# Performance work log

Measured on AMD Instinct MI355X. Metric: run time of the kernel, lower is better.

The kernel has to match this reference:

```python
import jax, jax.numpy as jnp
import numpy as np

# Bit-slice widths from SliceMethod([1,2,4]) on both input and weight sides
# (MSB-first, 7 magnitude bits total, sign carried per-element in each slice).
IN_SLICES = (1, 2, 4)
W_SLICES = (1, 2, 4)


def _l2norm(a):
    # F.normalize(a, p=2, dim=1)
    n = jnp.sqrt(jnp.sum(a * a, axis=1, keepdims=True))
    return a / jnp.maximum(n, 1e-12)


def _quantize(a, nbits):
    # symmetric fixed-point quantization to `nbits` magnitude bits,
    # dynamic per-tensor scale (bw_e=None -> fixed-point path)
    Q = float(2 ** nbits - 1)
    scale = jnp.max(jnp.abs(a))
    q = jnp.round(a / scale * Q)  # integer-valued float32 in [-Q, Q]
    return q, scale / Q


def _bit_slices(q, widths):
    # split |q| into bit groups (MSB-first per slice_method order); sign is
    # folded into each slice so recombination sum_k 2^off_k * slice_k == q
    sign = jnp.sign(q)
    mag = jnp.abs(q)
    total = sum(widths)
    slices = []
    off = total
    for w in widths:
        off -= w
        s = jnp.mod(jnp.floor(mag / (2.0 ** off)), 2.0 ** w)
        slices.append((sign * s, off))
    return slices


def setup_inputs() -> dict:
    key = jax.random.key(0)
    kx, kw = jax.random.split(key)
    x = jax.random.normal(kx, (4096, 1024), dtype=jnp.float32)
    weight = jax.random.normal(kw, (8192, 1024), dtype=jnp.float32)  # vectors.t -> [M, D]
    return {"x": x, "weight": weight}


def reference(x, weight):
    xn = _l2norm(x)        # [B, D]
    wn = _l2norm(weight)   # [M, D]
    qx, sx = _quantize(xn, sum(IN_SLICES))
    qw, sw = _quantize(wn, sum(W_SLICES))
    x_slices = _bit_slices(qx, IN_SLICES)
    w_slices = _bit_slices(qw, W_SLICES)
    # map_reduce_dot_func: 9 slice-pair low-bit GEMMs, recombined with 2^(oi+oj)
    acc = jnp.zeros((x.shape[0], weight.shape[0]), dtype=jnp.float32)
    for xs_k, ox in x_slices:
        for ws_k, ow in w_slices:
            acc = acc + (2.0 ** (ox + ow)) * jnp.einsum('bd,md->bm', xs_k, ws_k)
    cos = acc * sx * sw  # dequantize -> cosine similarity in [-1, 1]
    return 1.0 - cos
```

## Files before the change

kernel.cpp:

```cpp
#include <hip/hip_runtime.h>
#include <cstdint>
#include <cstddef>


#define D_COLS 1024
#define M_ROWS 4096
#define N_ROWS 8192

using i32x4 = __attribute__((ext_vector_type(4))) int;

__device__ __forceinline__ void gload_lds16(const void* g, void* lds) {
  __builtin_amdgcn_global_load_lds(
      (const __attribute__((address_space(1))) uint32_t*)g,
      (__attribute__((address_space(3))) uint32_t*)lds, 16, 0, 0);
}

__global__ __launch_bounds__(256) void rownorm_kernel(
    const float* __restrict__ x, const float* __restrict__ w,
    float* __restrict__ invnorm, float* __restrict__ rmax) {
  const int row = blockIdx.x;
  const float* a = (row < M_ROWS) ? x + (size_t)row * D_COLS
                                  : w + (size_t)(row - M_ROWS) * D_COLS;
  const float4 v = ((const float4*)a)[threadIdx.x];
  float ss = v.x * v.x + v.y * v.y + v.z * v.z + v.w * v.w;
  float mx = fmaxf(fmaxf(fabsf(v.x), fabsf(v.y)), fmaxf(fabsf(v.z), fabsf(v.w)));
#pragma unroll
  for (int off = 32; off; off >>= 1) {
    ss += __shfl_down(ss, off, 64);
    mx = fmaxf(mx, __shfl_down(mx, off, 64));
  }
  __shared__ float s_ss[4], s_mx[4];
  const int wave = threadIdx.x >> 6, lane = threadIdx.x & 63;
  if (lane == 0) { s_ss[wave] = ss; s_mx[wave] = mx; }
  __syncthreads();
  if (threadIdx.x == 0) {
    float tss = (s_ss[0] + s_ss[1]) + (s_ss[2] + s_ss[3]);
    float tmx = fmaxf(fmaxf(s_mx[0], s_mx[1]), fmaxf(s_mx[2], s_mx[3]));
    float inv = 1.0f / fmaxf(sqrtf(tss), 1e-12f);
    invnorm[row] = inv;
    rmax[row] = tmx * inv;
  }
}

__global__ __launch_bounds__(1024) void scale_reduce_kernel(
    const float* __restrict__ rmax, float* __restrict__ scales) {
  const int t = threadIdx.x;
  float mx = 0.f, mw = 0.f;
  for (int i = t; i < M_ROWS; i += 1024) mx = fmaxf(mx, rmax[i]);
  for (int i = t; i < N_ROWS; i += 1024) mw = fmaxf(mw, rmax[M_ROWS + i]);
#pragma unroll
  for (int off = 32; off; off >>= 1) {
    mx = fmaxf(mx, __shfl_down(mx, off, 64));
    mw = fmaxf(mw, __shfl_down(mw, off, 64));
  }
  __shared__ float smx[16], smw[16];
  const int wave = t >> 6, lane = t & 63;
  if (lane == 0) { smx[wave] = mx; smw[wave] = mw; }
  __syncthreads();
  if (t == 0) {
    float a = 0.f, b = 0.f;
#pragma unroll
    for (int i = 0; i < 16; ++i) { a = fmaxf(a, smx[i]); b = fmaxf(b, smw[i]); }
    scales[0] = a;
    scales[1] = b;
  }
}

__global__ __launch_bounds__(256) void quant_blocked_kernel(
    const float* __restrict__ a, const float* __restrict__ invnorm,
    const float* __restrict__ scale, uint4* __restrict__ img) {
  const int idx = blockIdx.x * 256 + threadIdx.x;
  const int rr = idx & 255;
  const int cc = (idx >> 8) & 63;
  const int p = idx >> 14;
  const int r = p * 256 + rr;
  const float f = invnorm[r] * (127.0f / scale[0]);
  const float4* src = (const float4*)(a + (size_t)r * D_COLS + cc * 16);
  unsigned pk[4];
#pragma unroll
  for (int q = 0; q < 4; ++q) {
    const float4 v = src[q];
    const int q0 = (int)rintf(v.x * f), q1 = (int)rintf(v.y * f);
    const int q2 = (int)rintf(v.z * f), q3 = (int)rintf(v.w * f);
    pk[q] = (unsigned)(q0 & 0xff) | ((unsigned)(q1 & 0xff) << 8) |
            ((unsigned)(q2 & 0xff) << 16) | ((unsigned)(q3 & 0xff) << 24);
  }
  img[idx] = make_uint4(pk[0], pk[1], pk[2], pk[3]);
}

__global__ __launch_bounds__(512, 2) void gemm_i8_kernel(
    const char* __restrict__ qx, const char* __restrict__ qw,
    const float* __restrict__ sx, const float* __restrict__ sw,
    float* __restrict__ out) {
  __shared__ __align__(16) char L[131072];
  const int t = threadIdx.x;
  const int wave = t >> 6, lane = t & 63;
  const int wr = wave >> 2, wc = wave & 3;
  const int rl = lane & 15, ko = lane >> 4;

  i32x4 acc[8][4] = {};

#define STAGE_TILE(pp, kt)                                                    \
  {                                                                           \
    const char* sa = qx + ((size_t)blockIdx.y * 8 + (kt)) * 32768;            \
    const char* sb = qw + ((size_t)blockIdx.x * 8 + (kt)) * 32768;            \
    _Pragma("unroll") for (int i = 0; i < 4; ++i) {                           \
      gload_lds16(sa + wave * 4096 + i * 1024 + lane * 16,                    \
                  L + (pp) * 65536 + wave * 4096 + i * 1024);                 \
      gload_lds16(sb + wave * 4096 + i * 1024 + lane * 16,                    \
                  L + (pp) * 65536 + 32768 + wave * 4096 + i * 1024);         \
    }                                                                         \
  }

  STAGE_TILE(0, 0);

#pragma unroll 1
  for (int kt = 0; kt < 8; ++kt) {
    const int p = kt & 1;
    asm volatile("s_waitcnt vmcnt(0) lgkmcnt(0)\n\ts_barrier" ::: "memory");
    __builtin_amdgcn_sched_barrier(0);
    if (kt < 7) STAGE_TILE(p ^ 1, kt + 1);
    __builtin_amdgcn_sched_barrier(0);

    const char* Ab = L + p * 65536;
    const char* Bb = L + p * 65536 + 32768;

#pragma unroll
    for (int qm = 0; qm < 2; ++qm) {
      i32x4 af[4][2];
#pragma unroll
      for (int m = 0; m < 4; ++m)
#pragma unroll
        for (int ks = 0; ks < 2; ++ks)
          af[m][ks] = *(const i32x4*)(Ab +
              ((ks * 4 + ko) * 256 + wr * 128 + (qm * 4 + m) * 16 + rl) * 16);
#pragma unroll
      for (int qn = 0; qn < 2; ++qn) {
        i32x4 bf[2][2];
#pragma unroll
        for (int n = 0; n < 2; ++n)
#pragma unroll
          for (int ks = 0; ks < 2; ++ks)
            bf[n][ks] = *(const i32x4*)(Bb +
                ((ks * 4 + ko) * 256 + wc * 64 + (qn * 2 + n) * 16 + rl) * 16);
        __builtin_amdgcn_s_barrier();
        __builtin_amdgcn_s_setprio(1);
#pragma unroll
        for (int ks = 0; ks < 2; ++ks)
#pragma unroll
          for (int m = 0; m < 4; ++m)
#pragma unroll
            for (int n = 0; n < 2; ++n)
              acc[qm * 4 + m][qn * 2 + n] = __builtin_amdgcn_mfma_i32_16x16x64_i8(
                  af[m][ks], bf[n][ks], acc[qm * 4 + m][qn * 2 + n], 0, 0, 0);
        __builtin_amdgcn_s_setprio(0);
        __builtin_amdgcn_s_barrier();
      }
    }
  }
#undef STAGE_TILE

  const float cs = sx[0] * sw[0] * (1.0f / 16129.0f);
  const int rowBase = blockIdx.y * 256;
  const int colBase = blockIdx.x * 256;
#pragma unroll
  for (int m = 0; m < 8; ++m) {
    const int row = rowBase + wr * 128 + m * 16 + ko * 4;
#pragma unroll
    for (int n = 0; n < 4; ++n) {
      const int col = colBase + wc * 64 + n * 16 + rl;
#pragma unroll
      for (int j = 0; j < 4; ++j)
        out[(size_t)(row + j) * N_ROWS + col] = 1.0f - (float)acc[m][n][j] * cs;
    }
  }
}

extern "C" void kernel_launch(void* const* d_in, const int* in_sizes, int n_in,
                              void* d_out, int out_size, void* d_ws, size_t ws_size,
                              hipStream_t stream) {
  const float* x = (const float*)d_in[0];
  const float* w = (const float*)d_in[1];
  float* out = (float*)d_out;

  char* ws = (char*)d_ws;
  char* qx = ws;
  char* qw = ws + (size_t)M_ROWS * D_COLS;
  float* invnorm = (float*)(ws + (size_t)(M_ROWS + N_ROWS) * D_COLS);
  float* rmax = invnorm + (M_ROWS + N_ROWS);
  float* scales = rmax + (M_ROWS + N_ROWS);

  rownorm_kernel<<<M_ROWS + N_ROWS, 256, 0, stream>>>(x, w, invnorm, rmax);
  scale_reduce_kernel<<<1, 1024, 0, stream>>>(rmax, scales);

  quant_blocked_kernel<<<M_ROWS * (D_COLS / 16) / 256, 256, 0, stream>>>(
      x, invnorm, &scales[0], (uint4*)qx);
  quant_blocked_kernel<<<N_ROWS * (D_COLS / 16) / 256, 256, 0, stream>>>(
      w, invnorm + M_ROWS, &scales[1], (uint4*)qw);

  dim3 grid(N_ROWS / 256, M_ROWS / 256);
  gemm_i8_kernel<<<grid, 512, 0, stream>>>(qx, qw, &scales[0], &scales[1], out);
}
```

Measured before the change: 90.96 us.

## Replace double-buffered K tiles with 4-slot half-tile ring prefetching 3 ahead

Splits each 128-wide K tile into two 64-wide half-tiles and stages them in a 4-slot LDS ring, issuing global-to-LDS loads three half-tiles ahead. Each phase waits with a counted vmcnt, so only the current half-tile must have landed rather than draining all loads as the old double-buffered loop did. The aim is to keep memory traffic in flight across barriers and overlap it better with the MFMA work. In exchange there are twice as many barrier phases, and the ring relies on the trailing barrier to keep a slot from being overwritten while other waves are still reading it.

```diff
diff --git a/kernel.cpp b/kernel.cpp
--- a/kernel.cpp
+++ b/kernel.cpp
@@ -100,65 +100,51 @@
 
   i32x4 acc[8][4] = {};
 
-#define STAGE_TILE(pp, kt)                                                    \
+#define ISSUE_HT(h)                                                           \
   {                                                                           \
-    const char* sa = qx + ((size_t)blockIdx.y * 8 + (kt)) * 32768;            \
-    const char* sb = qw + ((size_t)blockIdx.x * 8 + (kt)) * 32768;            \
-    _Pragma("unroll") for (int i = 0; i < 4; ++i) {                           \
-      gload_lds16(sa + wave * 4096 + i * 1024 + lane * 16,                    \
-                  L + (pp) * 65536 + wave * 4096 + i * 1024);                 \
-      gload_lds16(sb + wave * 4096 + i * 1024 + lane * 16,                    \
-                  L + (pp) * 65536 + 32768 + wave * 4096 + i * 1024);         \
+    const int kt_ = (h) >> 1, ks_ = (h) & 1, bb_ = (h) & 3;                   \
+    const char* sa_ = qx + ((size_t)blockIdx.y * 8 + kt_) * 32768 + ks_ * 16384; \
+    const char* sb_ = qw + ((size_t)blockIdx.x * 8 + kt_) * 32768 + ks_ * 16384; \
+    _Pragma("unroll") for (int i_ = 0; i_ < 2; ++i_) {                        \
+      gload_lds16(sa_ + wave * 2048 + i_ * 1024 + lane * 16,                  \
+                  L + bb_ * 32768 + wave * 2048 + i_ * 1024);                 \
+      gload_lds16(sb_ + wave * 2048 + i_ * 1024 + lane * 16,                  \
+                  L + bb_ * 32768 + 16384 + wave * 2048 + i_ * 1024);         \
     }                                                                         \
   }
 
-  STAGE_TILE(0, 0);
+#define PHASE(h, VM)                                                          \
+  {                                                                           \
+    if ((h) + 3 < 16) ISSUE_HT((h) + 3);                                      \
+    asm volatile("s_waitcnt vmcnt(" #VM ")" ::: "memory");                    \
+    asm volatile("s_barrier" ::: "memory");                                   \
+    const char* Ab_ = L + ((h) & 3) * 32768;                                  \
+    const char* Bb_ = Ab_ + 16384;                                            \
+    i32x4 af_[8], bf_[4];                                                     \
+    _Pragma("unroll") for (int m_ = 0; m_ < 8; ++m_)                          \
+      af_[m_] = *(const i32x4*)(Ab_ + (ko * 256 + wr * 128 + m_ * 16 + rl) * 16); \
+    _Pragma("unroll") for (int n_ = 0; n_ < 4; ++n_)                          \
+      bf_[n_] = *(const i32x4*)(Bb_ + (ko * 256 + wc * 64 + n_ * 16 + rl) * 16); \
+    __builtin_amdgcn_s_setprio(1);                                            \
+    _Pragma("unroll") for (int m_ = 0; m_ < 8; ++m_)                          \
+      _Pragma("unroll") for (int n_ = 0; n_ < 4; ++n_)                        \
+        acc[m_][n_] = __builtin_amdgcn_mfma_i32_16x16x64_i8(                  \
+            af_[m_], bf_[n_], acc[m_][n_], 0, 0, 0);                          \
+    __builtin_amdgcn_s_setprio(0);                                            \
+    asm volatile("s_barrier" ::: "memory");                                   \
+  }
+
+  ISSUE_HT(0);
+  ISSUE_HT(1);
+  ISSUE_HT(2);
 
 #pragma unroll 1
-  for (int kt = 0; kt < 8; ++kt) {
-    const int p = kt & 1;
-    asm volatile("s_waitcnt vmcnt(0) lgkmcnt(0)\n\ts_barrier" ::: "memory");
-    __builtin_amdgcn_sched_barrier(0);
-    if (kt < 7) STAGE_TILE(p ^ 1, kt + 1);
-    __builtin_amdgcn_sched_barrier(0);
-
-    const char* Ab = L + p * 65536;
-    const char* Bb = L + p * 65536 + 32768;
-
-#pragma unroll
-    for (int qm = 0; qm < 2; ++qm) {
-      i32x4 af[4][2];
-#pragma unroll
-      for (int m = 0; m < 4; ++m)
-#pragma unroll
-        for (int ks = 0; ks < 2; ++ks)
-          af[m][ks] = *(const i32x4*)(Ab +
-              ((ks * 4 + ko) * 256 + wr * 128 + (qm * 4 + m) * 16 + rl) * 16);
-#pragma unroll
-      for (int qn = 0; qn < 2; ++qn) {
-        i32x4 bf[2][2];
-#pragma unroll
-        for (int n = 0; n < 2; ++n)
-#pragma unroll
-          for (int ks = 0; ks < 2; ++ks)
-            bf[n][ks] = *(const i32x4*)(Bb +
-                ((ks * 4 + ko) * 256 + wc * 64 + (qn * 2 + n) * 16 + rl) * 16);
-        __builtin_amdgcn_s_barrier();
-        __builtin_amdgcn_s_setprio(1);
-#pragma unroll
-        for (int ks = 0; ks < 2; ++ks)
-#pragma unroll
-          for (int m = 0; m < 4; ++m)
-#pragma unroll
-            for (int n = 0; n < 2; ++n)
-              acc[qm * 4 + m][qn * 2 + n] = __builtin_amdgcn_mfma_i32_16x16x64_i8(
-                  af[m][ks], bf[n][ks], acc[qm * 4 + m][qn * 2 + n], 0, 0, 0);
-        __builtin_amdgcn_s_setprio(0);
-        __builtin_amdgcn_s_barrier();
-      }
-    }
-  }
-#undef STAGE_TILE
+  for (int h = 0; h < 13; ++h) PHASE(h, 12);
+  PHASE(13, 8);
+  PHASE(14, 4);
+  PHASE(15, 0);
+#undef PHASE
+#undef ISSUE_HT
 
   const float cs = sx[0] * sw[0] * (1.0f / 16129.0f);
   const int rowBase = blockIdx.y * 256;
```

After: 88.17 us. -3.1%, faster.
